# Kernel tuning notes

Measured on AMD Instinct MI355X. Metric: run time of the kernel, lower is better.

Reference implementation:

```python
import jax, jax.numpy as jnp
import numpy as np

B, S, H, NH, BS = 1, 4096, 1024, 16, 64  # batch, seq, hidden, heads, block_size
HD = H // NH                             # head_dim = 64
SPARSITY = 0.9


def _block_sparse_mask():
    # Mirrors SparseAttention._compute_block_mask: random block mask * upper-tri,
    # expanded by block_size. Diagonal blocks forced on so no row is fully masked.
    nb = S // BS
    rng = np.random.default_rng(0)
    keep = rng.random((nb, nb)) > SPARSITY
    tri = np.triu(np.ones((nb, nb), dtype=bool))
    bm = (keep & tri) | np.eye(nb, dtype=bool)
    full = np.repeat(np.repeat(bm, BS, axis=0), BS, axis=1)  # [S,S]
    return jnp.asarray(full[None, None])                     # [1,1,S,S]


def setup_inputs() -> dict:
    key = jax.random.key(0)
    ks = jax.random.split(key, 5)
    std = 0.02
    return {
        "hidden_states": jax.random.normal(ks[0], (B, S, H), dtype=jnp.float32),
        "wq": jax.random.normal(ks[1], (H, H), dtype=jnp.float32) * std,
        "bq": jnp.zeros((H,), dtype=jnp.float32),
        "wk": jax.random.normal(ks[2], (H, H), dtype=jnp.float32) * std,
        "bk": jnp.zeros((H,), dtype=jnp.float32),
        "wv": jax.random.normal(ks[3], (H, H), dtype=jnp.float32) * std,
        "bv": jnp.zeros((H,), dtype=jnp.float32),
        "wo": jax.random.normal(ks[4], (H, H), dtype=jnp.float32) * std,
        "bo": jnp.zeros((H,), dtype=jnp.float32),
        "attention_mask": _block_sparse_mask(),
    }


def reference(hidden_states, wq, bq, wk, bk, wv, bv, wo, bo, attention_mask):
    b, s, h = hidden_states.shape
    scaling = HD ** -0.5

    def split_heads(x):  # [B,S,H] -> [B,NH,S,HD]
        return x.reshape(b, s, NH, HD).transpose(0, 2, 1, 3)

    q = split_heads(hidden_states @ wq.T + bq)
    k = split_heads(hidden_states @ wk.T + bk)
    v = split_heads(hidden_states @ wv.T + bv)

    scores = jnp.einsum("bhqd,bhkd->bhqk", q, k) * scaling  # [B,NH,S,S]
    scores = jnp.where(attention_mask, scores, -jnp.inf)
    probs = jax.nn.softmax(scores, axis=-1)  # dropout is identity in eval
    attn = jnp.einsum("bhqk,bhkd->bhqd", probs, v)
    attn = attn.transpose(0, 2, 1, 3).reshape(b, s, h)
    return attn @ wo.T + bo
```

## Files before the change

kernel.cpp:

```cpp
#include <hip/hip_runtime.h>
#include <hip/hip_bf16.h>
#include <stdint.h>

#define SEQ   4096
#define HID   1024
#define NHEAD 16
#define HD    64
#define NBLK  64
#define KSTR  72

typedef __bf16 bf16;
typedef __bf16 bf16x8 __attribute__((ext_vector_type(8)));
typedef __bf16 bf16x4 __attribute__((ext_vector_type(4)));
typedef float  floatx4 __attribute__((ext_vector_type(4)));

__device__ __forceinline__ void gl_lds16(const void* g, void* l) {
  __builtin_amdgcn_global_load_lds(
      (const __attribute__((address_space(1))) void*)g,
      (__attribute__((address_space(3))) void*)l, 16, 0, 0);
}

__device__ __forceinline__ int detect_f32(const void* p) {
  unsigned wv = ((const unsigned*)p)[threadIdx.x & 63];
  unsigned ex = ((wv & 0xFFFFu) >> 7) & 0xFFu;
  unsigned long long b = __ballot(ex >= 140u);
  return __popcll(b) >= 8;
}

__global__ __launch_bounds__(256) void convert_inputs(
    const void* hs, const void* wq, const void* wk, const void* wv, const void* wo,
    const void* bq, const void* bk, const void* bv, const void* bo, bf16* dst)
{
  int f32 = detect_f32(hs);
  int blk = blockIdx.x, t = threadIdx.x;

  if (blk == 2048) {
#pragma unroll
    for (int j = 0; j < 4; ++j) {
      int c = j * 256 + t;
      int which = c >> 8, lc = c & 255;
      const void* bsrc = (which == 0) ? bq : (which == 1) ? bk : (which == 2) ? bv : bo;
      size_t doff = (which == 0) ? 5242880u : (which == 1) ? 6292480u
                   : (which == 2) ? 7342080u : 8391680u;
      bf16x4 v;
      if (f32) {
        const float* s = (const float*)bsrc + lc * 4;
        v[0] = (bf16)s[0]; v[1] = (bf16)s[1]; v[2] = (bf16)s[2]; v[3] = (bf16)s[3];
      } else v = *(const bf16x4*)((const bf16*)bsrc + lc * 4);
      *(bf16x4*)(dst + doff + lc * 4) = v;
    }
    return;
  }

  const void* src; size_t doff; int lb;
  if (blk < 1024)      { src = hs; doff = 0;        lb = blk; }
  else if (blk < 1280) { src = wq; doff = 4194304u; lb = blk - 1024; }
  else if (blk < 1536) { src = wk; doff = 5243904u; lb = blk - 1280; }
  else if (blk < 1792) { src = wv; doff = 6293504u; lb = blk - 1536; }
  else                 { src = wo; doff = 7343104u; lb = blk - 1792; }

#pragma unroll
  for (int j = 0; j < 4; ++j) {
    size_t c = (size_t)lb * 1024 + j * 256 + t;
    bf16x4 v;
    if (f32) {
      const float* s = (const float*)src + c * 4;
      v[0] = (bf16)s[0]; v[1] = (bf16)s[1]; v[2] = (bf16)s[2]; v[3] = (bf16)s[3];
    } else v = *(const bf16x4*)((const bf16*)src + c * 4);
    *(bf16x4*)(dst + doff + c * 4) = v;
  }
}

__device__ __forceinline__ void gemm128_body(
    const bf16* __restrict__ A, const bf16* __restrict__ Bw,
    const bf16* __restrict__ bias, void* __restrict__ Cout,
    float scale, int mode, int f32out, char* smem)
{
  const int K = HID, N = HID;
  int bn = blockIdx.x, bm = blockIdx.y;
  int t = threadIdx.x;
  int w = t >> 6, lane = t & 63;
  int wm = w >> 1, wn = w & 1;
  int lr = lane & 15, lq = lane >> 4;

  floatx4 acc[4][4] = {};

  const bf16* Ab = A  + (size_t)bm * 128 * K;
  const bf16* Bb = Bw + (size_t)bn * 128 * K;

  int ci0 = t, ci1 = t + 256;
  int r0 = ci0 >> 2, c0 = (ci0 & 3) * 8;
  int r1 = ci1 >> 2, c1 = (ci1 & 3) * 8;

  {
    bf16* As = (bf16*)smem; bf16* Bs = (bf16*)(smem + 16384);
    gl_lds16(Ab + (size_t)r0 * K + c0, As + ci0 * 8);
    gl_lds16(Ab + (size_t)r1 * K + c1, As + ci1 * 8);
    gl_lds16(Bb + (size_t)r0 * K + c0, Bs + ci0 * 8);
    gl_lds16(Bb + (size_t)r1 * K + c1, Bs + ci1 * 8);
  }

  int cur = 0;
  for (int k0 = 0; k0 < K; k0 += 32) {
    __syncthreads();

    if (k0 + 32 < K) {
      int nb = cur ^ 1;
      bf16* As = (bf16*)(smem + nb * 8192);
      bf16* Bs = (bf16*)(smem + 16384 + nb * 8192);
      gl_lds16(Ab + (size_t)r0 * K + k0 + 32 + c0, As + ci0 * 8);
      gl_lds16(Ab + (size_t)r1 * K + k0 + 32 + c1, As + ci1 * 8);
      gl_lds16(Bb + (size_t)r0 * K + k0 + 32 + c0, Bs + ci0 * 8);
      gl_lds16(Bb + (size_t)r1 * K + k0 + 32 + c1, Bs + ci1 * 8);
    }

    const bf16* As = (const bf16*)(smem + cur * 8192);
    const bf16* Bs = (const bf16*)(smem + 16384 + cur * 8192);
    bf16x8 af[4], bfv[4];
#pragma unroll
    for (int i = 0; i < 4; ++i) {
      af[i]  = *(const bf16x8*)(As + (wm * 64 + i * 16 + lr) * 32 + lq * 8);
      bfv[i] = *(const bf16x8*)(Bs + (wn * 64 + i * 16 + lr) * 32 + lq * 8);
    }
#pragma unroll
    for (int mi = 0; mi < 4; ++mi)
#pragma unroll
      for (int ni = 0; ni < 4; ++ni)
        acc[mi][ni] = __builtin_amdgcn_mfma_f32_16x16x32_bf16(
            af[mi], bfv[ni], acc[mi][ni], 0, 0, 0);

    cur ^= 1;
  }

  float* Ew = (float*)smem + w * 16 * 68;
  int head = bn * 2 + wn;
#pragma unroll
  for (int mi = 0; mi < 4; ++mi) {
    __syncthreads();
#pragma unroll
    for (int ni = 0; ni < 4; ++ni) {
      int colg = bn * 128 + wn * 64 + ni * 16 + lr;
      float bv = (float)bias[colg];
#pragma unroll
      for (int r = 0; r < 4; ++r)
        Ew[(lq * 4 + r) * 68 + ni * 16 + lr] = (acc[mi][ni][r] + bv) * scale;
    }
    __syncthreads();
#pragma unroll
    for (int hh = 0; hh < 4; ++hh) {
      int s_loc = (lane >> 4) + hh * 4;
      int c4 = (lane & 15) * 4;
      floatx4 v = *(const floatx4*)&Ew[s_loc * 68 + c4];
      int row = bm * 128 + wm * 64 + mi * 16 + s_loc;
      if (mode == 1) {
        bf16x4 pk; pk[0] = (bf16)v[0]; pk[1] = (bf16)v[1]; pk[2] = (bf16)v[2]; pk[3] = (bf16)v[3];
        *(bf16x4*)&((bf16*)Cout)[(size_t)head * SEQ * HD + (size_t)row * HD + c4] = pk;
      } else if (f32out) {
        *(floatx4*)&((float*)Cout)[(size_t)row * N + bn * 128 + wn * 64 + c4] = v;
      } else {
        bf16x4 pk; pk[0] = (bf16)v[0]; pk[1] = (bf16)v[1]; pk[2] = (bf16)v[2]; pk[3] = (bf16)v[3];
        *(bf16x4*)&((bf16*)Cout)[(size_t)row * N + bn * 128 + wn * 64 + c4] = pk;
      }
    }
  }
}

__global__ __launch_bounds__(256) void gemm_qkv_kernel(
    const bf16* __restrict__ X,
    const bf16* __restrict__ wq, const bf16* __restrict__ wk, const bf16* __restrict__ wv,
    const bf16* __restrict__ bq, const bf16* __restrict__ bk, const bf16* __restrict__ bv,
    bf16* __restrict__ Q, bf16* __restrict__ K, bf16* __restrict__ Vh)
{
  __shared__ __align__(16) char smem[32768];
  int z = blockIdx.z;
  const bf16* W = (z == 0) ? wq : (z == 1) ? wk : wv;
  const bf16* b = (z == 0) ? bq : (z == 1) ? bk : bv;
  bf16* O = (z == 0) ? Q : (z == 1) ? K : Vh;
  float scale = (z == 0) ? 0.125f : 1.0f;
  gemm128_body(X, W, b, O, scale, 1, 0, smem);
}

__global__ __launch_bounds__(256) void gemm_out_kernel(
    const bf16* __restrict__ A, const bf16* __restrict__ W,
    const bf16* __restrict__ b, void* __restrict__ O, const void* hs_raw)
{
  __shared__ __align__(16) char smem[32768];
  int f32o = detect_f32(hs_raw);
  gemm128_body(A, W, b, O, 1.0f, 0, f32o, smem);
}

__global__ __launch_bounds__(256) void transpose_v(
    const bf16* __restrict__ Vh, bf16* __restrict__ Vt)
{
  int h = blockIdx.y, sb = blockIdx.x;
  __shared__ __align__(16) bf16 T[64 * KSTR];
  int t = threadIdx.x;
  const bf16* Vb = Vh + (size_t)h * SEQ * HD + (size_t)sb * 64 * HD;
#pragma unroll
  for (int it = 0; it < 2; ++it) {
    int s = (t >> 3) + it * 32;
    int d0 = (t & 7) * 8;
    bf16x8 v = *(const bf16x8*)&Vb[(size_t)s * HD + d0];
#pragma unroll
    for (int j = 0; j < 8; ++j)
      T[(d0 + j) * KSTR + s] = v[j];
  }
  __syncthreads();
  bf16* Vo = Vt + (size_t)h * HD * SEQ + (size_t)sb * 64;
#pragma unroll
  for (int it = 0; it < 2; ++it) {
    int d = (t >> 3) + it * 32;
    int s0 = (t & 7) * 8;
    bf16x8 v = *(const bf16x8*)&T[d * KSTR + s0];
    *(bf16x8*)&Vo[(size_t)d * SEQ + s0] = v;
  }
}

__global__ __launch_bounds__(256) void sparse_attn(
    const bf16* __restrict__ Qh, const bf16* __restrict__ Kh,
    const bf16* __restrict__ Vt, const void* __restrict__ mask,
    bf16* __restrict__ attn_out)
{
  int qb = blockIdx.x, h = blockIdx.y;
  int t = threadIdx.x, w = t >> 6, lane = t & 63;
  int lr = lane & 15, lq = lane >> 4;

  __shared__ __align__(16) bf16 Ks[2][64 * 64];
  __shared__ __align__(16) bf16 Vs[2][64 * 64];
  __shared__ __align__(16) bf16 Pl[4 * 16 * KSTR];
  __shared__ int s_cnt;
  __shared__ int s_list[64];
  bf16* Pw = Pl + w * 16 * KSTR;

  if (t < 64) {
    unsigned w0 = ((const unsigned*)mask)[0], w1 = ((const unsigned*)mask)[1];
    int f;
    if (w0 == 0x01010101u)                  f = 1;
    else if (w0 == 0x3F803F80u)             f = 2;
    else if (w0 == 0x3C003C00u)             f = 2;
    else if (w0 == 0x3F800000u)             f = 3;
    else if (w0 == 1u && w1 == 1u)          f = 0;
    else if (w0 == 1u && w1 == 0u)          f = 4;
    else if (w0 == 0u && w1 == 0x3FF00000u) f = 5;
    else f = 0;
    size_t e = (size_t)qb * 64 * SEQ + (size_t)t * 64;
    bool kept;
    switch (f) {
      case 1: kept = ((const unsigned char*)mask)[e] != 0; break;
      case 2: kept = ((const unsigned short*)mask)[e] != 0; break;
      case 3: kept = ((const unsigned*)mask)[e] != 0; break;
      case 4:
      case 5: kept = ((const unsigned long long*)mask)[e] != 0ull; break;
      default: kept = ((const int*)mask)[e] != 0; break;
    }
    unsigned long long b = __ballot(kept);
    if (kept) s_list[__popcll(b & ((1ull << t) - 1ull))] = t;
    if (t == 0) s_cnt = (int)__popcll(b);
  }
  __syncthreads();
  int n = s_cnt;

  const bf16* Qbase = Qh + (size_t)h * SEQ * HD;
  const bf16* Kbase = Kh + (size_t)h * SEQ * HD;
  const bf16* Vtb   = Vt + (size_t)h * HD * SEQ;

  bf16x8 qf[2];
#pragma unroll
  for (int ks = 0; ks < 2; ++ks)
    qf[ks] = *(const bf16x8*)&Qbase[(size_t)(qb * 64 + w * 16 + lr) * HD + ks * 32 + lq * 8];

  floatx4 o_acc[4] = {};
  float l_lane[4] = {0.f, 0.f, 0.f, 0.f};

  int ci0 = t, ci1 = t + 256;
  int r0 = ci0 >> 3, g0 = (ci0 & 7) ^ (r0 & 7);
  int r1 = ci1 >> 3, g1 = (ci1 & 7) ^ (r1 & 7);

  {
    int kb = s_list[0];
    const bf16* Kblk = Kbase + (size_t)kb * (64 * HD);
    const bf16* Vblk = Vtb + (size_t)kb * 64;
    gl_lds16(Kblk + (size_t)r0 * HD + g0 * 8, &Ks[0][ci0 * 8]);
    gl_lds16(Kblk + (size_t)r1 * HD + g1 * 8, &Ks[0][ci1 * 8]);
    gl_lds16(Vblk + (size_t)r0 * SEQ + g0 * 8, &Vs[0][ci0 * 8]);
    gl_lds16(Vblk + (size_t)r1 * SEQ + g1 * 8, &Vs[0][ci1 * 8]);
  }

  int rsw = lr & 7;
  int cur = 0;
  for (int it = 0; it < n; ++it) {
    __syncthreads();

    if (it + 1 < n) {
      int kb2 = s_list[it + 1];
      const bf16* Kblk = Kbase + (size_t)kb2 * (64 * HD);
      const bf16* Vblk = Vtb + (size_t)kb2 * 64;
      int nb = cur ^ 1;
      gl_lds16(Kblk + (size_t)r0 * HD + g0 * 8, &Ks[nb][ci0 * 8]);
      gl_lds16(Kblk + (size_t)r1 * HD + g1 * 8, &Ks[nb][ci1 * 8]);
      gl_lds16(Vblk + (size_t)r0 * SEQ + g0 * 8, &Vs[nb][ci0 * 8]);
      gl_lds16(Vblk + (size_t)r1 * SEQ + g1 * 8, &Vs[nb][ci1 * 8]);
    }

    floatx4 s_acc[4] = {};
#pragma unroll
    for (int ks = 0; ks < 2; ++ks)
#pragma unroll
      for (int ni = 0; ni < 4; ++ni) {
        int cs = (ks * 4 + lq) ^ rsw;
        bf16x8 kf = *(const bf16x8*)&Ks[cur][(ni * 16 + lr) * 64 + cs * 8];
        s_acc[ni] = __builtin_amdgcn_mfma_f32_16x16x32_bf16(qf[ks], kf, s_acc[ni], 0, 0, 0);
      }

#pragma unroll
    for (int ni = 0; ni < 4; ++ni)
#pragma unroll
      for (int r = 0; r < 4; ++r) {
        float p = __expf(s_acc[ni][r] - 3.0f);
        s_acc[ni][r] = p;
        l_lane[r] += p;
      }

#pragma unroll
    for (int ni = 0; ni < 4; ++ni)
#pragma unroll
      for (int r = 0; r < 4; ++r)
        Pw[(lq * 4 + r) * KSTR + ni * 16 + lr] = (bf16)s_acc[ni][r];

    bf16x8 pf[2];
#pragma unroll
    for (int ks = 0; ks < 2; ++ks)
      pf[ks] = *(const bf16x8*)&Pw[lr * KSTR + ks * 32 + lq * 8];

#pragma unroll
    for (int ks = 0; ks < 2; ++ks)
#pragma unroll
      for (int ni = 0; ni < 4; ++ni) {
        int cs = (ks * 4 + lq) ^ rsw;
        bf16x8 vfr = *(const bf16x8*)&Vs[cur][(ni * 16 + lr) * 64 + cs * 8];
        o_acc[ni] = __builtin_amdgcn_mfma_f32_16x16x32_bf16(pf[ks], vfr, o_acc[ni], 0, 0, 0);
      }

    cur ^= 1;
  }

  float l_row[4];
#pragma unroll
  for (int r = 0; r < 4; ++r) {
    float s = l_lane[r];
#pragma unroll
    for (int d = 1; d < 16; d <<= 1) s += __shfl_xor(s, d, 64);
    l_row[r] = s;
  }

#pragma unroll
  for (int ni = 0; ni < 4; ++ni)
#pragma unroll
    for (int r = 0; r < 4; ++r) {
      int row = qb * 64 + w * 16 + lq * 4 + r;
      int col = h * 64 + ni * 16 + lr;
      attn_out[(size_t)row * HID + col] = (bf16)(o_acc[ni][r] / l_row[r]);
    }
}

extern "C" void kernel_launch(void* const* d_in, const int* in_sizes, int n_in,
                              void* d_out, int out_size, void* d_ws, size_t ws_size,
                              hipStream_t stream)
{
  const void* hs = d_in[0];
  const void* wq = d_in[1];
  const void* bq = d_in[2];
  const void* wk = d_in[3];
  const void* bk = d_in[4];
  const void* wv = d_in[5];
  const void* bv = d_in[6];
  const void* wo = d_in[7];
  const void* bo = d_in[8];
  const void* mask = d_in[9];

  char* ws = (char*)d_ws;
  const size_t SZ = (size_t)NHEAD * SEQ * HD;
  bf16* conv = (bf16*)ws;
  bf16* hs_b = conv;
  bf16* wq_b = conv + 4194304;
  bf16* bq_b = conv + 5242880;
  bf16* wk_b = conv + 5243904;
  bf16* bk_b = conv + 6292480;
  bf16* wv_b = conv + 6293504;
  bf16* bv_b = conv + 7342080;
  bf16* wo_b = conv + 7343104;
  bf16* bo_b = conv + 8391680;
  bf16* Q  = conv + 8392704;
  bf16* Kh = Q  + SZ;
  bf16* Vt = Kh + SZ;
  bf16* At = Vt + SZ;
  bf16* Vh = At;

  convert_inputs<<<2049, 256, 0, stream>>>(hs, wq, wk, wv, wo, bq, bk, bv, bo, conv);
  gemm_qkv_kernel<<<dim3(8, 32, 3), 256, 0, stream>>>(hs_b, wq_b, wk_b, wv_b,
                                                      bq_b, bk_b, bv_b, Q, Kh, Vh);
  transpose_v<<<dim3(NBLK, NHEAD), 256, 0, stream>>>(Vh, Vt);
  sparse_attn<<<dim3(NBLK, NHEAD), 256, 0, stream>>>(Q, Kh, Vt, mask, At);
  gemm_out_kernel<<<dim3(8, 32), 256, 0, stream>>>(At, wo_b, bo_b, d_out, hs);
}
```

Measured before the change: 219.0 us.

## Fuse V transpose into QKV GEMM epilogue and shrink P staging buffer

The QKV GEMM now writes V directly in transposed [head][d][seq] layout through a new epilogue mode, so the separate transpose_v kernel and its launch and round trip through global memory are removed. In attention, P is staged to LDS one 32-column half at a time with a smaller stride, which reduces the LDS footprint and interleaves the write/read with the PV MFMAs. The transposed epilogue performs scalar LDS reads and 16-byte global stores strided by SEQ, which may coalesce less well than the old row stores.

```diff
diff --git a/kernel.cpp b/kernel.cpp
--- a/kernel.cpp
+++ b/kernel.cpp
@@ -7,7 +7,7 @@
 #define NHEAD 16
 #define HD    64
 #define NBLK  64
-#define KSTR  72
+#define PSTR  36
 
 typedef __bf16 bf16;
 typedef __bf16 bf16x8 __attribute__((ext_vector_type(8)));
@@ -146,20 +146,33 @@
         Ew[(lq * 4 + r) * 68 + ni * 16 + lr] = (acc[mi][ni][r] + bv) * scale;
     }
     __syncthreads();
-#pragma unroll
-    for (int hh = 0; hh < 4; ++hh) {
-      int s_loc = (lane >> 4) + hh * 4;
-      int c4 = (lane & 15) * 4;
-      floatx4 v = *(const floatx4*)&Ew[s_loc * 68 + c4];
-      int row = bm * 128 + wm * 64 + mi * 16 + s_loc;
-      if (mode == 1) {
-        bf16x4 pk; pk[0] = (bf16)v[0]; pk[1] = (bf16)v[1]; pk[2] = (bf16)v[2]; pk[3] = (bf16)v[3];
-        *(bf16x4*)&((bf16*)Cout)[(size_t)head * SEQ * HD + (size_t)row * HD + c4] = pk;
-      } else if (f32out) {
-        *(floatx4*)&((float*)Cout)[(size_t)row * N + bn * 128 + wn * 64 + c4] = v;
-      } else {
-        bf16x4 pk; pk[0] = (bf16)v[0]; pk[1] = (bf16)v[1]; pk[2] = (bf16)v[2]; pk[3] = (bf16)v[3];
-        *(bf16x4*)&((bf16*)Cout)[(size_t)row * N + bn * 128 + wn * 64 + c4] = pk;
+    if (mode == 2) {
+      int d = lane;
+      int row0 = bm * 128 + wm * 64 + mi * 16;
+      bf16x8 p0, p1;
+#pragma unroll
+      for (int s = 0; s < 8; ++s)  p0[s] = (bf16)Ew[s * 68 + d];
+#pragma unroll
+      for (int s = 0; s < 8; ++s)  p1[s] = (bf16)Ew[(s + 8) * 68 + d];
+      bf16* dst = (bf16*)Cout + (size_t)head * HD * SEQ + (size_t)d * SEQ + row0;
+      *(bf16x8*)dst = p0;
+      *(bf16x8*)(dst + 8) = p1;
+    } else {
+#pragma unroll
+      for (int hh = 0; hh < 4; ++hh) {
+        int s_loc = (lane >> 4) + hh * 4;
+        int c4 = (lane & 15) * 4;
+        floatx4 v = *(const floatx4*)&Ew[s_loc * 68 + c4];
+        int row = bm * 128 + wm * 64 + mi * 16 + s_loc;
+        if (mode == 1) {
+          bf16x4 pk; pk[0] = (bf16)v[0]; pk[1] = (bf16)v[1]; pk[2] = (bf16)v[2]; pk[3] = (bf16)v[3];
+          *(bf16x4*)&((bf16*)Cout)[(size_t)head * SEQ * HD + (size_t)row * HD + c4] = pk;
+        } else if (f32out) {
+          *(floatx4*)&((float*)Cout)[(size_t)row * N + bn * 128 + wn * 64 + c4] = v;
+        } else {
+          bf16x4 pk; pk[0] = (bf16)v[0]; pk[1] = (bf16)v[1]; pk[2] = (bf16)v[2]; pk[3] = (bf16)v[3];
+          *(bf16x4*)&((bf16*)Cout)[(size_t)row * N + bn * 128 + wn * 64 + c4] = pk;
+        }
       }
     }
   }
@@ -169,15 +182,16 @@
     const bf16* __restrict__ X,
     const bf16* __restrict__ wq, const bf16* __restrict__ wk, const bf16* __restrict__ wv,
     const bf16* __restrict__ bq, const bf16* __restrict__ bk, const bf16* __restrict__ bv,
-    bf16* __restrict__ Q, bf16* __restrict__ K, bf16* __restrict__ Vh)
+    bf16* __restrict__ Q, bf16* __restrict__ K, bf16* __restrict__ Vt)
 {
   __shared__ __align__(16) char smem[32768];
   int z = blockIdx.z;
   const bf16* W = (z == 0) ? wq : (z == 1) ? wk : wv;
   const bf16* b = (z == 0) ? bq : (z == 1) ? bk : bv;
-  bf16* O = (z == 0) ? Q : (z == 1) ? K : Vh;
+  bf16* O = (z == 0) ? Q : (z == 1) ? K : Vt;
   float scale = (z == 0) ? 0.125f : 1.0f;
-  gemm128_body(X, W, b, O, scale, 1, 0, smem);
+  int mode = (z == 2) ? 2 : 1;
+  gemm128_body(X, W, b, O, scale, mode, 0, smem);
 }
 
 __global__ __launch_bounds__(256) void gemm_out_kernel(
@@ -187,33 +201,6 @@
   __shared__ __align__(16) char smem[32768];
   int f32o = detect_f32(hs_raw);
   gemm128_body(A, W, b, O, 1.0f, 0, f32o, smem);
-}
-
-__global__ __launch_bounds__(256) void transpose_v(
-    const bf16* __restrict__ Vh, bf16* __restrict__ Vt)
-{
-  int h = blockIdx.y, sb = blockIdx.x;
-  __shared__ __align__(16) bf16 T[64 * KSTR];
-  int t = threadIdx.x;
-  const bf16* Vb = Vh + (size_t)h * SEQ * HD + (size_t)sb * 64 * HD;
-#pragma unroll
-  for (int it = 0; it < 2; ++it) {
-    int s = (t >> 3) + it * 32;
-    int d0 = (t & 7) * 8;
-    bf16x8 v = *(const bf16x8*)&Vb[(size_t)s * HD + d0];
-#pragma unroll
-    for (int j = 0; j < 8; ++j)
-      T[(d0 + j) * KSTR + s] = v[j];
-  }
-  __syncthreads();
-  bf16* Vo = Vt + (size_t)h * HD * SEQ + (size_t)sb * 64;
-#pragma unroll
-  for (int it = 0; it < 2; ++it) {
-    int d = (t >> 3) + it * 32;
-    int s0 = (t & 7) * 8;
-    bf16x8 v = *(const bf16x8*)&T[d * KSTR + s0];
-    *(bf16x8*)&Vo[(size_t)d * SEQ + s0] = v;
-  }
 }
 
 __global__ __launch_bounds__(256) void sparse_attn(
@@ -227,10 +214,10 @@
 
   __shared__ __align__(16) bf16 Ks[2][64 * 64];
   __shared__ __align__(16) bf16 Vs[2][64 * 64];
-  __shared__ __align__(16) bf16 Pl[4 * 16 * KSTR];
+  __shared__ __align__(16) bf16 Pl[4 * 16 * PSTR];
   __shared__ int s_cnt;
   __shared__ int s_list[64];
-  bf16* Pw = Pl + w * 16 * KSTR;
+  bf16* Pw = Pl + w * 16 * PSTR;
 
   if (t < 64) {
     unsigned w0 = ((const unsigned*)mask)[0], w1 = ((const unsigned*)mask)[1];
@@ -322,24 +309,20 @@
       }
 
 #pragma unroll
-    for (int ni = 0; ni < 4; ++ni)
-#pragma unroll
-      for (int r = 0; r < 4; ++r)
-        Pw[(lq * 4 + r) * KSTR + ni * 16 + lr] = (bf16)s_acc[ni][r];
-
-    bf16x8 pf[2];
-#pragma unroll
-    for (int ks = 0; ks < 2; ++ks)
-      pf[ks] = *(const bf16x8*)&Pw[lr * KSTR + ks * 32 + lq * 8];
-
-#pragma unroll
-    for (int ks = 0; ks < 2; ++ks)
+    for (int ks = 0; ks < 2; ++ks) {
+#pragma unroll
+      for (int ni = 0; ni < 2; ++ni)
+#pragma unroll
+        for (int r = 0; r < 4; ++r)
+          Pw[(lq * 4 + r) * PSTR + ni * 16 + lr] = (bf16)s_acc[ks * 2 + ni][r];
+      bf16x8 pf = *(const bf16x8*)&Pw[lr * PSTR + lq * 8];
 #pragma unroll
       for (int ni = 0; ni < 4; ++ni) {
         int cs = (ks * 4 + lq) ^ rsw;
         bf16x8 vfr = *(const bf16x8*)&Vs[cur][(ni * 16 + lr) * 64 + cs * 8];
-        o_acc[ni] = __builtin_amdgcn_mfma_f32_16x16x32_bf16(pf[ks], vfr, o_acc[ni], 0, 0, 0);
+        o_acc[ni] = __builtin_amdgcn_mfma_f32_16x16x32_bf16(pf, vfr, o_acc[ni], 0, 0, 0);
       }
+    }
 
     cur ^= 1;
   }
@@ -394,12 +377,10 @@
   bf16* Kh = Q  + SZ;
   bf16* Vt = Kh + SZ;
   bf16* At = Vt + SZ;
-  bf16* Vh = At;
 
   convert_inputs<<<2049, 256, 0, stream>>>(hs, wq, wk, wv, wo, bq, bk, bv, bo, conv);
   gemm_qkv_kernel<<<dim3(8, 32, 3), 256, 0, stream>>>(hs_b, wq_b, wk_b, wv_b,
-                                                      bq_b, bk_b, bv_b, Q, Kh, Vh);
-  transpose_v<<<dim3(NBLK, NHEAD), 256, 0, stream>>>(Vh, Vt);
+                                                      bq_b, bk_b, bv_b, Q, Kh, Vt);
   sparse_attn<<<dim3(NBLK, NHEAD), 256, 0, stream>>>(Q, Kh, Vt, mask, At);
   gemm_out_kernel<<<dim3(8, 32), 256, 0, stream>>>(At, wo_b, bo_b, d_out, hs);
 }
```

Result: slower. 230.5 us (+5.2%).
